# Optimization experiments

Measured on AMD Instinct MI355X. Metric: run time of the kernel, lower is better.

Reference implementation:

```python
import jax, jax.numpy as jnp
import numpy as np

B, N, D, H, P = 8, 1025, 768, 12, 32  # n = P*P + 1 (CLS + patches)
HD = D // H
EPS = 1e-5


def setup_inputs() -> dict:
    key = jax.random.key(0)
    ks = jax.random.split(key, 6)
    return {
        "x": jax.random.normal(ks[0], (B, N, D), dtype=jnp.float32),
        "canny": jax.random.uniform(ks[1], (B, 1, P, P), dtype=jnp.float32),
        "noise": jax.random.uniform(ks[2], (B, P, P), dtype=jnp.float32),
        "ln_w": jnp.ones((D,), dtype=jnp.float32),
        "ln_b": jnp.zeros((D,), dtype=jnp.float32),
        "w_qkv": (jax.random.normal(ks[3], (D, 3 * D), dtype=jnp.float32) * 0.02),
        "w_out": (jax.random.normal(ks[4], (D, D), dtype=jnp.float32) * 0.02),
        "b_out": jnp.zeros((D,), dtype=jnp.float32),
    }


def reference(x, canny, noise, ln_w, ln_b, w_qkv, w_out, b_out):
    b, n, d = x.shape
    # LayerNorm
    mu = jnp.mean(x, axis=-1, keepdims=True)
    var = jnp.mean(jnp.square(x - mu), axis=-1, keepdims=True)
    x_norm = (x - mu) * jax.lax.rsqrt(var + EPS) * ln_w + ln_b
    # QKV projection (no bias), split into heads: [b, n, 3, h, hd]
    qkv = (x_norm @ w_qkv).reshape(b, n, 3, H, HD)
    q = jnp.transpose(qkv[:, :, 0], (0, 2, 1, 3))  # [b, h, n, hd]
    k = jnp.transpose(qkv[:, :, 1], (0, 2, 1, 3))
    v = jnp.transpose(qkv[:, :, 2], (0, 2, 1, 3))
    # NOTE: source uses scale = dim ** -0.5 (full dim, not head_dim)
    dots = jnp.einsum('bhid,bhjd->bhij', q, k) * (d ** -0.5)
    # CLS-row prior injection: softmax over patch keys of CLS query row
    attn_row = jax.nn.softmax(dots[:, :, 0, 1:], axis=-1)  # [b, h, n-1]
    canny_flat = canny.reshape(b, -1) + 1.0                # [b, n-1]
    canny_flat = canny_flat / jnp.sum(canny_flat, axis=-1, keepdims=True)
    noise_flat = noise.reshape(b, -1)                      # [b, n-1]
    noise_flat = noise_flat / jnp.sum(noise_flat, axis=-1, keepdims=True)
    attn_row = attn_row + canny_flat[:, None, :] + noise_flat[:, None, :]
    dots = dots.at[:, :, 0, 1:].set(attn_row)
    # Second (full) softmax; dropout is identity in eval mode
    attn = jax.nn.softmax(dots, axis=-1)
    out = jnp.einsum('bhij,bhjd->bhid', attn, v)           # [b, h, n, hd]
    out = jnp.transpose(out, (0, 2, 1, 3)).reshape(b, n, d)
    return out @ w_out + b_out
```

## Files before the change

### kernel.cpp

```cpp
#include <hip/hip_runtime.h>

#define B_ 8
#define N_ 1025
#define D_ 768
#define H_ 12
#define NP_ 1024
#define ROWS_ (B_*N_)
#define ROWS_PAD_ 8320
#define QKVC_ 2304
#define SCALE_ 0.03608439182435161f
#define EPS_ 1e-5f

typedef float f32x4 __attribute__((ext_vector_type(4)));
typedef short s16x8 __attribute__((ext_vector_type(8)));

#define GLD16(g, l) __builtin_amdgcn_global_load_lds( \
    (const __attribute__((address_space(1))) unsigned int*)(g), \
    (__attribute__((address_space(3))) unsigned int*)(l), 16, 0, 0)

__device__ __forceinline__ float blo(unsigned int u){
  union { unsigned int i; float f; } v; v.i = u << 16; return v.f;
}
__device__ __forceinline__ float bhi(unsigned int u){
  union { unsigned int i; float f; } v; v.i = u & 0xffff0000u; return v.f;
}
__device__ __forceinline__ float bf2f(unsigned short u){
  union { unsigned int i; float f; } v; v.i = ((unsigned int)u) << 16; return v.f;
}
__device__ __forceinline__ unsigned short f2bf(float f){
  union { unsigned int i; float f; } v; v.f = f;
  unsigned int b = v.i;
  b = b + 0x7fffu + ((b >> 16) & 1u);
  return (unsigned short)(b >> 16);
}
__device__ __forceinline__ unsigned int pkbf2(float a, float b){
  union { float f; unsigned int i; } ua, ub;
  ua.f = a; ub.f = b;
  return __builtin_amdgcn_perm(ub.i + 0x8000u, ua.i + 0x8000u, 0x07060302u);
}

__global__ __launch_bounds__(256) void prep_fused(
    const float* __restrict__ w1, unsigned short* __restrict__ d1,
    const float* __restrict__ w2, unsigned short* __restrict__ d2,
    const float* __restrict__ x, const float* __restrict__ lw,
    const float* __restrict__ lb, unsigned short* __restrict__ xn) {
  int id = blockIdx.x;
  int t = threadIdx.x;
  if (id < 2304) {
    __shared__ unsigned short tile[32][33];
    int bx = id % 96;
    int kb = (id / 96) * 32;
    const float* src; unsigned short* dst; int N, nb;
    if (bx < 72) { src = w1; dst = d1; N = QKVC_; nb = bx * 32; }
    else         { src = w2; dst = d2; N = D_;    nb = (bx - 72) * 32; }
    int tx = t & 31, ty = t >> 5;
    #pragma unroll
    for (int i = 0; i < 4; i++) {
      int r = ty + i * 8;
      tile[r][tx] = f2bf(src[(size_t)(kb + r) * N + nb + tx]);
    }
    __syncthreads();
    #pragma unroll
    for (int i = 0; i < 4; i++) {
      int r = ty + i * 8;
      dst[(size_t)(nb + r) * D_ + kb + tx] = tile[tx][r];
    }
  } else {
    int row = id - 2304;
    __shared__ float r6[6];
    float4 v; float s = 0.f, q = 0.f;
    if (t < 192) {
      v = ((const float4*)(x + (size_t)row * D_))[t];
      s = v.x + v.y + v.z + v.w;
      q = v.x * v.x + v.y * v.y + v.z * v.z + v.w * v.w;
      #pragma unroll
      for (int off = 32; off > 0; off >>= 1) {
        s += __shfl_xor(s, off, 64);
        q += __shfl_xor(q, off, 64);
      }
      if ((t & 63) == 0) { r6[t >> 6] = s; r6[3 + (t >> 6)] = q; }
    }
    __syncthreads();
    if (t < 192) {
      s = r6[0] + r6[1] + r6[2];
      q = r6[3] + r6[4] + r6[5];
      float mean = s * (1.0f / 768.0f);
      float var = q * (1.0f / 768.0f) - mean * mean;
      var = var < 0.f ? 0.f : var;
      float rstd = rsqrtf(var + EPS_);
      float4 wv4 = ((const float4*)lw)[t];
      float4 bv4 = ((const float4*)lb)[t];
      float o0 = (v.x - mean) * rstd * wv4.x + bv4.x;
      float o1 = (v.y - mean) * rstd * wv4.y + bv4.y;
      float o2 = (v.z - mean) * rstd * wv4.z + bv4.z;
      float o3 = (v.w - mean) * rstd * wv4.w + bv4.w;
      uint2 pk = {pkbf2(o0, o1), pkbf2(o2, o3)};
      *(uint2*)(xn + (size_t)row * D_ + t * 4) = pk;
    }
  }
}

template <bool OF32>
__global__ __launch_bounds__(256) void gemm_bt(
    const unsigned short* __restrict__ A, const unsigned short* __restrict__ Bt,
    void* __restrict__ Cv, const float* __restrict__ bias,
    int Mvalid, int Nn, int Kk) {
  __shared__ short sh[32768];
  int t = threadIdx.x;
  int lane = t & 63, w = t >> 6;
  int m16 = lane & 15, quad = lane >> 4;

  int nwg = gridDim.x;
  int nbx = Nn >> 7;
  int id = blockIdx.x;
  int qq = nwg >> 3, rr = nwg & 7;
  int xcd = id & 7, off = id >> 3;
  int wg = (xcd < rr ? xcd * (qq + 1) : rr * (qq + 1) + (xcd - rr) * qq) + off;
  int bx = wg % nbx, by = wg / nbx;
  int bm = by * 128, bn = bx * 128;

  int wm = (w & 1) * 64, wn = (w >> 1) * 64;

  f32x4 acc[4][4];
  #pragma unroll
  for (int i = 0; i < 4; i++)
    #pragma unroll
    for (int j = 0; j < 4; j++) acc[i][j] = (f32x4){0.f, 0.f, 0.f, 0.f};

  const unsigned short* aP[4];
  const unsigned short* bP[4];
  #pragma unroll
  for (int c = 0; c < 4; c++) {
    int g = t + c * 256;
    int row = g >> 3, slot = g & 7;
    aP[c] = A  + (size_t)(bm + row) * Kk + ((slot ^ (row & 7)) * 8);
    bP[c] = Bt + (size_t)(bn + row) * Kk + ((slot ^ (row & 7)) * 8);
  }

  int KS = Kk >> 6;
  int cur = 0;
  #pragma unroll
  for (int c = 0; c < 4; c++) GLD16(aP[c], sh + (t + c * 256) * 8);
  #pragma unroll
  for (int c = 0; c < 4; c++) GLD16(bP[c], sh + 16384 + (t + c * 256) * 8);

  for (int kt = 0; kt < KS; kt++) {
    asm volatile("s_waitcnt vmcnt(0)" ::: "memory");
    __builtin_amdgcn_s_barrier();
    if (kt + 1 < KS) {
      int nb2 = (cur ^ 1) * 8192;
      int ko = (kt + 1) * 64;
      #pragma unroll
      for (int c = 0; c < 4; c++) GLD16(aP[c] + ko, sh + nb2 + (t + c * 256) * 8);
      #pragma unroll
      for (int c = 0; c < 4; c++) GLD16(bP[c] + ko, sh + 16384 + nb2 + (t + c * 256) * 8);
    }
    const short* sa = sh + cur * 8192;
    const short* sb = sh + 16384 + cur * 8192;
    #pragma unroll
    for (int ks = 0; ks < 2; ks++) {
      int so = ((ks * 4 + quad) ^ (m16 & 7)) * 8;
      s16x8 af[4], bfr[4];
      #pragma unroll
      for (int i = 0; i < 4; i++) {
        af[i]  = *(const s16x8*)(sa + (wm + i * 16 + m16) * 64 + so);
        bfr[i] = *(const s16x8*)(sb + (wn + i * 16 + m16) * 64 + so);
      }
      __builtin_amdgcn_s_setprio(1);
      #pragma unroll
      for (int i = 0; i < 4; i++)
        #pragma unroll
        for (int j = 0; j < 4; j++)
          acc[i][j] = __builtin_amdgcn_mfma_f32_16x16x32_bf16(af[i], bfr[j], acc[i][j], 0, 0, 0);
      __builtin_amdgcn_s_setprio(0);
    }
    cur ^= 1;
  }
  __syncthreads();

  if (!OF32) {
    unsigned short* C = (unsigned short*)Cv;
    #pragma unroll
    for (int j = 0; j < 4; j++) {
      int col = wn + j * 16 + m16;
      #pragma unroll
      for (int i = 0; i < 4; i++)
        #pragma unroll
        for (int r = 0; r < 4; r++)
          sh[(wm + i * 16 + quad * 4 + r) * 128 + col] = (short)f2bf(acc[i][j][r]);
    }
    __syncthreads();
    #pragma unroll
    for (int c = 0; c < 8; c++) {
      int idx = c * 256 + t;
      int row = idx >> 4, col = (idx & 15) * 8;
      if (bm + row < Mvalid)
        *(uint4*)(&C[(size_t)(bm + row) * Nn + bn + col]) = *(const uint4*)(&sh[row * 128 + col]);
    }
  } else {
    float* Cf = (float*)Cv;
    float* shf = (float*)sh;
    #pragma unroll
    for (int j = 0; j < 4; j++) {
      int col = wn + j * 16 + m16;
      float bv = bias ? bias[bn + col] : 0.f;
      #pragma unroll
      for (int i = 0; i < 4; i++)
        #pragma unroll
        for (int r = 0; r < 4; r++)
          shf[(wm + i * 16 + quad * 4 + r) * 128 + col] = acc[i][j][r] + bv;
    }
    __syncthreads();
    #pragma unroll
    for (int c = 0; c < 16; c++) {
      int idx = c * 256 + t;
      int row = idx >> 5, col = (idx & 31) * 4;
      if (bm + row < Mvalid)
        *(float4*)(&Cf[(size_t)(bm + row) * Nn + bn + col]) =
            *(const float4*)(&shf[row * 128 + col]);
    }
  }
}

__device__ __forceinline__ float block_sum(float v, float* red) {
  int t = threadIdx.x;
  red[t] = v;
  __syncthreads();
  for (int st = 128; st > 0; st >>= 1) {
    if (t < st) red[t] += red[t + st];
    __syncthreads();
  }
  float r = red[0];
  __syncthreads();
  return r;
}

__global__ __launch_bounds__(256) void attn_fused(
    const unsigned short* __restrict__ qkv, const float* __restrict__ canny,
    const float* __restrict__ noise, unsigned short* __restrict__ attn_out) {
  __shared__ __align__(16) char pool[37888];
  int id = blockIdx.x;
  int t = threadIdx.x;

  if (id < 768) {
    short* ps = (short*)pool;
    short* ks = (short*)(pool + 18432);
    unsigned int* vs = (unsigned int*)(pool + 27648);
    float* tailbuf = (float*)(pool + 36864);

    int tile = id / 96;
    int rem = id % 96;
    int h = rem >> 3;
    int b = rem & 7;
    int lane = t & 63, w = t >> 6;
    int m16 = lane & 15, quad = lane >> 4;

    int qbase = 1 + tile * 128;

    {
      int r = t >> 1, seg = (t & 1) * 32;
      const uint4* src = (const uint4*)(qkv + (size_t)(b * N_ + qbase + r) * QKVC_ + h * 64 + seg);
      uint4 u0 = src[0], u1 = src[1], u2 = src[2], u3 = src[3];
      *(uint4*)(&ps[r * 72 + seg])      = u0;
      *(uint4*)(&ps[r * 72 + seg + 8])  = u1;
      *(uint4*)(&ps[r * 72 + seg + 16]) = u2;
      *(uint4*)(&ps[r * 72 + seg + 24]) = u3;
    }
    s16x8 qb[2][2];
    #pragma unroll
    for (int nt = 0; nt < 2; nt++)
      #pragma unroll
      for (int ks_ = 0; ks_ < 2; ks_++) {
        qb[nt][ks_] = *(const s16x8*)(&ps[(w * 32 + nt * 16 + m16) * 72 + ks_ * 32 + quad * 8]);
        unsigned int* u = (unsigned int*)&qb[nt][ks_];
        #pragma unroll
        for (int i = 0; i < 4; i++)
          u[i] = pkbf2(blo(u[i]) * SCALE_, bhi(u[i]) * SCALE_);
      }
    s16x8 vone;
    #pragma unroll
    for (int i = 0; i < 8; i++) vone[i] = (short)0x3F80;

    f32x4 oacc[2][4], lacc[2];
    #pragma unroll
    for (int mt = 0; mt < 2; mt++) {
      lacc[mt] = (f32x4){0.f, 0.f, 0.f, 0.f};
      #pragma unroll
      for (int dt = 0; dt < 4; dt++) oacc[mt][dt] = (f32x4){0.f, 0.f, 0.f, 0.f};
    }

    int kkey = t >> 2, kseg = (t & 3) * 16;
    const unsigned short* kbase = qkv + (size_t)(b * N_) * QKVC_ + D_ + h * 64;
    int vp2 = t & 31, vseg = t >> 5;
    const unsigned short* vbase = qkv + (size_t)(b * N_) * QKVC_ + 2 * D_ + h * 64 + vseg * 8;
    uint4 kr0, kr1, vr0, vr1;
    {
      const uint4* ksrc = (const uint4*)(kbase + (size_t)kkey * QKVC_ + kseg);
      kr0 = ksrc[0]; kr1 = ksrc[1];
      vr0 = *(const uint4*)(vbase + (size_t)(2 * vp2) * QKVC_);
      vr1 = *(const uint4*)(vbase + (size_t)(2 * vp2 + 1) * QKVC_);
    }

    for (int jt = 0; jt < 16; jt++) {
      __syncthreads();
      *(uint4*)(&ks[kkey * 72 + kseg])     = kr0;
      *(uint4*)(&ks[kkey * 72 + kseg + 8]) = kr1;
      {
        const unsigned int* vaw = (const unsigned int*)&vr0;
        const unsigned int* vbw = (const unsigned int*)&vr1;
        #pragma unroll
        for (int i = 0; i < 4; i++) {
          vs[(vseg * 8 + 2 * i)     * 36 + vp2] = __builtin_amdgcn_perm(vbw[i], vaw[i], 0x05040100u);
          vs[(vseg * 8 + 2 * i + 1) * 36 + vp2] = __builtin_amdgcn_perm(vbw[i], vaw[i], 0x07060302u);
        }
      }
      __syncthreads();
      if (jt < 15) {
        int j0 = (jt + 1) * 64;
        const uint4* ksrc = (const uint4*)(kbase + (size_t)(j0 + kkey) * QKVC_ + kseg);
        kr0 = ksrc[0]; kr1 = ksrc[1];
        vr0 = *(const uint4*)(vbase + (size_t)(j0 + 2 * vp2) * QKVC_);
        vr1 = *(const uint4*)(vbase + (size_t)(j0 + 2 * vp2 + 1) * QKVC_);
      }
      f32x4 sacc[4][2];
      #pragma unroll
      for (int kt = 0; kt < 4; kt++) {
        s16x8 ka0 = *(const s16x8*)(&ks[(kt * 16 + m16) * 72 + quad * 8]);
        s16x8 ka1 = *(const s16x8*)(&ks[(kt * 16 + m16) * 72 + 32 + quad * 8]);
        #pragma unroll
        for (int nt = 0; nt < 2; nt++) {
          f32x4 s = (f32x4){0.f, 0.f, 0.f, 0.f};
          s = __builtin_amdgcn_mfma_f32_16x16x32_bf16(ka0, qb[nt][0], s, 0, 0, 0);
          s = __builtin_amdgcn_mfma_f32_16x16x32_bf16(ka1, qb[nt][1], s, 0, 0, 0);
          sacc[kt][nt] = s;
        }
      }
      #pragma unroll
      for (int kt = 0; kt < 4; kt++) {
        #pragma unroll
        for (int nt = 0; nt < 2; nt++) {
          f32x4 s = sacc[kt][nt];
          float p0 = __expf(s[0]);
          float p1 = __expf(s[1]);
          float p2 = __expf(s[2]);
          float p3 = __expf(s[3]);
          uint2 pk = {pkbf2(p0, p1), pkbf2(p2, p3)};
          *(uint2*)(&ps[(w * 32 + nt * 16 + m16) * 72 + kt * 16 + quad * 4]) = pk;
        }
      }
      __syncthreads();
      s16x8 pa[2][2];
      #pragma unroll
      for (int mt = 0; mt < 2; mt++)
        #pragma unroll
        for (int ks_ = 0; ks_ < 2; ks_++)
          pa[mt][ks_] = *(const s16x8*)(&ps[(w * 32 + mt * 16 + m16) * 72 + ks_ * 32 + quad * 8]);
      const short* vss = (const short*)vs;
      #pragma unroll
      for (int dt = 0; dt < 4; dt++) {
        s16x8 vb0 = *(const s16x8*)(&vss[(dt * 16 + m16) * 72 + quad * 8]);
        s16x8 vb1 = *(const s16x8*)(&vss[(dt * 16 + m16) * 72 + 32 + quad * 8]);
        #pragma unroll
        for (int mt = 0; mt < 2; mt++) {
          oacc[mt][dt] = __builtin_amdgcn_mfma_f32_16x16x32_bf16(pa[mt][0], vb0, oacc[mt][dt], 0, 0, 0);
          oacc[mt][dt] = __builtin_amdgcn_mfma_f32_16x16x32_bf16(pa[mt][1], vb1, oacc[mt][dt], 0, 0, 0);
        }
      }
      #pragma unroll
      for (int mt = 0; mt < 2; mt++) {
        lacc[mt] = __builtin_amdgcn_mfma_f32_16x16x32_bf16(pa[mt][0], vone, lacc[mt], 0, 0, 0);
        lacc[mt] = __builtin_amdgcn_mfma_f32_16x16x32_bf16(pa[mt][1], vone, lacc[mt], 0, 0, 0);
      }
    }
    if (t < 64)       tailbuf[t]             = bf2f(qkv[(size_t)(b * N_ + 1024) * QKVC_ + D_     + h * 64 + t]);
    else if (t < 128) tailbuf[64 + (t - 64)] = bf2f(qkv[(size_t)(b * N_ + 1024) * QKVC_ + 2 * D_ + h * 64 + (t - 64)]);
    __syncthreads();
    #pragma unroll
    for (int nt = 0; nt < 2; nt++) {
      float d = 0.f;
      #pragma unroll
      for (int jj = 0; jj < 8; jj++) {
        d += bf2f((unsigned short)qb[nt][0][jj]) * tailbuf[quad * 8 + jj];
        d += bf2f((unsigned short)qb[nt][1][jj]) * tailbuf[32 + quad * 8 + jj];
      }
      d += __shfl_xor(d, 16, 64);
      d += __shfl_xor(d, 32, 64);
      float p = __expf(d);
      if (quad == 0) tailbuf[128 + w * 32 + nt * 16 + m16] = p;
    }
    __syncthreads();
    #pragma unroll
    for (int mt = 0; mt < 2; mt++)
      #pragma unroll
      for (int r = 0; r < 4; r++) {
        float pr = tailbuf[128 + w * 32 + mt * 16 + quad * 4 + r];
        lacc[mt][r] += pr;
        #pragma unroll
        for (int dt = 0; dt < 4; dt++)
          oacc[mt][dt][r] += pr * tailbuf[64 + dt * 16 + m16];
      }
    #pragma unroll
    for (int mt = 0; mt < 2; mt++) {
      float rinv[4];
      #pragma unroll
      for (int r = 0; r < 4; r++) rinv[r] = 1.0f / lacc[mt][r];
      #pragma unroll
      for (int dt = 0; dt < 4; dt++) {
        #pragma unroll
        for (int r = 0; r < 4; r++) {
          int grow = b * N_ + qbase + w * 32 + mt * 16 + quad * 4 + r;
          attn_out[(size_t)grow * D_ + h * 64 + dt * 16 + m16] = f2bf(oacc[mt][dt][r] * rinv[r]);
        }
      }
    }
  } else {
    float* s     = (float*)pool;
    float* red   = (float*)(pool + 4608);
    float* q     = (float*)(pool + 5632);
    float* pvred = (float*)(pool + 5888);

    int bh = id - 768;
    int b = bh / H_, h = bh % H_;

    if (t < 64) q[t] = bf2f(qkv[(size_t)(b * N_) * QKVC_ + h * 64 + t]);
    __syncthreads();

    for (int j = t; j < N_; j += 256) {
      const unsigned short* krow = qkv + (size_t)(b * N_ + j) * QKVC_ + D_ + h * 64;
      float dot = 0.f;
      #pragma unroll
      for (int c = 0; c < 8; c++) {
        uint4 kk = *(const uint4*)(krow + c * 8);
        dot += q[c*8+0]*blo(kk.x) + q[c*8+1]*bhi(kk.x)
             + q[c*8+2]*blo(kk.y) + q[c*8+3]*bhi(kk.y)
             + q[c*8+4]*blo(kk.z) + q[c*8+5]*bhi(kk.z)
             + q[c*8+6]*blo(kk.w) + q[c*8+7]*bhi(kk.w);
      }
      s[j] = dot * SCALE_;
    }
    float cp = 0.f, npp = 0.f;
    for (int j = t; j < NP_; j += 256) {
      cp  += canny[b * NP_ + j] + 1.0f;
      npp += noise[b * NP_ + j];
    }
    float csum = block_sum(cp, red);
    float nsum = block_sum(npp, red);
    float e1 = 0.f;
    for (int j = t; j < N_; j += 256) if (j >= 1) e1 += __expf(s[j]);
    float sum1 = block_sum(e1, red);
    for (int j = t; j < N_; j += 256) {
      if (j >= 1) {
        s[j] = __expf(s[j]) / sum1
             + (canny[b * NP_ + j - 1] + 1.0f) / csum
             + noise[b * NP_ + j - 1] / nsum;
      }
    }
    __syncthreads();
    float e2 = 0.f;
    for (int j = t; j < N_; j += 256) { float e = __expf(s[j]); s[j] = e; e2 += e; }
    float sum2 = block_sum(e2, red);
    {
      int o = t & 7, g = t >> 3;
      float a[8] = {0.f, 0.f, 0.f, 0.f, 0.f, 0.f, 0.f, 0.f};
      for (int j = g; j < N_; j += 32) {
        float sv = s[j];
        uint4 vv = *(const uint4*)(qkv + (size_t)(b * N_ + j) * QKVC_ + 2 * D_ + h * 64 + o * 8);
        a[0] += sv * blo(vv.x); a[1] += sv * bhi(vv.x);
        a[2] += sv * blo(vv.y); a[3] += sv * bhi(vv.y);
        a[4] += sv * blo(vv.z); a[5] += sv * bhi(vv.z);
        a[6] += sv * blo(vv.w); a[7] += sv * bhi(vv.w);
      }
      #pragma unroll
      for (int i = 0; i < 8; i++) pvred[(o * 8 + i) * 33 + g] = a[i];
    }
    __syncthreads();
    if (t < 64) {
      float acc = 0.f;
      #pragma unroll
      for (int u = 0; u < 32; u++) acc += pvred[t * 33 + u];
      attn_out[(size_t)(b * N_) * D_ + h * 64 + t] = f2bf(acc / sum2);
    }
  }
}

extern "C" void kernel_launch(void* const* d_in, const int* in_sizes, int n_in,
                              void* d_out, int out_size, void* d_ws, size_t ws_size,
                              hipStream_t stream) {
  (void)in_sizes; (void)n_in; (void)out_size; (void)ws_size;
  const float* x     = (const float*)d_in[0];
  const float* canny = (const float*)d_in[1];
  const float* noise = (const float*)d_in[2];
  const float* lnw   = (const float*)d_in[3];
  const float* lnb   = (const float*)d_in[4];
  const float* wqkv  = (const float*)d_in[5];
  const float* wout  = (const float*)d_in[6];
  const float* bout  = (const float*)d_in[7];
  float* out = (float*)d_out;
  char* ws = (char*)d_ws;

  unsigned short* xn    = (unsigned short*)(ws);
  unsigned short* wqkvT = (unsigned short*)(ws + 12779520);
  unsigned short* woutT = (unsigned short*)(ws + 16318464);
  unsigned short* qkv   = (unsigned short*)(ws + 17498112);

  prep_fused<<<dim3(2304 + ROWS_), 256, 0, stream>>>(
      wqkv, wqkvT, wout, woutT, x, lnw, lnb, xn);
  gemm_bt<false><<<dim3((QKVC_ / 128) * (ROWS_PAD_ / 128)), 256, 0, stream>>>(
      xn, wqkvT, (void*)qkv, nullptr, ROWS_, QKVC_, D_);
  attn_fused<<<dim3(768 + B_ * H_), 256, 0, stream>>>(qkv, canny, noise, xn);
  gemm_bt<true><<<dim3((D_ / 128) * (ROWS_PAD_ / 128)), 256, 0, stream>>>(
      xn, woutT, (void*)out, bout, ROWS_, D_, D_);
}
```

Measured before the change: 205.4 us.

## Widen GEMM tiles to 128x256 with 8 waves and BK=32 staging

The bf16 GEMM kernel now uses 512 threads (8 waves) computing a 128x256 output tile instead of 256 threads on 128x128. K-step staging drops from 64 to 32, with a 4-slot XOR swizzle to fit the larger B tile in a smaller LDS buffer. The epilogue is split into halves or quarters to reuse the reduced shared memory. This is meant to improve A-tile reuse and per-block MFMA density. The costs are half as many workgroups, which matters for the 768-wide output projection, and twice as many barrier iterations along K.

```diff
diff --git a/kernel.cpp b/kernel.cpp
--- a/kernel.cpp
+++ b/kernel.cpp
@@ -101,25 +101,25 @@
 }
 
 template <bool OF32>
-__global__ __launch_bounds__(256) void gemm_bt(
+__global__ __launch_bounds__(512) void gemm_bt(
     const unsigned short* __restrict__ A, const unsigned short* __restrict__ Bt,
     void* __restrict__ Cv, const float* __restrict__ bias,
     int Mvalid, int Nn, int Kk) {
-  __shared__ short sh[32768];
+  __shared__ short sh[24576];
   int t = threadIdx.x;
   int lane = t & 63, w = t >> 6;
   int m16 = lane & 15, quad = lane >> 4;
 
   int nwg = gridDim.x;
-  int nbx = Nn >> 7;
+  int nbx = Nn >> 8;
   int id = blockIdx.x;
   int qq = nwg >> 3, rr = nwg & 7;
   int xcd = id & 7, off = id >> 3;
   int wg = (xcd < rr ? xcd * (qq + 1) : rr * (qq + 1) + (xcd - rr) * qq) + off;
   int bx = wg % nbx, by = wg / nbx;
-  int bm = by * 128, bn = bx * 128;
-
-  int wm = (w & 1) * 64, wn = (w >> 1) * 64;
+  int bm = by * 128, bn = bx * 256;
+
+  int wm = (w >> 2) * 64, wn = (w & 3) * 64;
 
   f32x4 acc[4][4];
   #pragma unroll
@@ -127,97 +127,100 @@
     #pragma unroll
     for (int j = 0; j < 4; j++) acc[i][j] = (f32x4){0.f, 0.f, 0.f, 0.f};
 
-  const unsigned short* aP[4];
-  const unsigned short* bP[4];
-  #pragma unroll
-  for (int c = 0; c < 4; c++) {
-    int g = t + c * 256;
-    int row = g >> 3, slot = g & 7;
-    aP[c] = A  + (size_t)(bm + row) * Kk + ((slot ^ (row & 7)) * 8);
-    bP[c] = Bt + (size_t)(bn + row) * Kk + ((slot ^ (row & 7)) * 8);
-  }
-
-  int KS = Kk >> 6;
+  int srow = t >> 2;
+  int sxor = ((t & 3) ^ (srow & 3)) * 8;
+  const unsigned short* aP  = A  + (size_t)(bm + srow) * Kk + sxor;
+  const unsigned short* bP0 = Bt + (size_t)(bn + srow) * Kk + sxor;
+  const unsigned short* bP1 = Bt + (size_t)(bn + 128 + srow) * Kk + sxor;
+
+  int KS = Kk >> 5;
   int cur = 0;
-  #pragma unroll
-  for (int c = 0; c < 4; c++) GLD16(aP[c], sh + (t + c * 256) * 8);
-  #pragma unroll
-  for (int c = 0; c < 4; c++) GLD16(bP[c], sh + 16384 + (t + c * 256) * 8);
-
+  GLD16(aP,  sh + t * 8);
+  GLD16(bP0, sh + 4096 + t * 8);
+  GLD16(bP1, sh + 4096 + (t + 512) * 8);
+
+  int so = (quad ^ (m16 & 3)) * 8;
   for (int kt = 0; kt < KS; kt++) {
     asm volatile("s_waitcnt vmcnt(0)" ::: "memory");
     __builtin_amdgcn_s_barrier();
     if (kt + 1 < KS) {
-      int nb2 = (cur ^ 1) * 8192;
-      int ko = (kt + 1) * 64;
-      #pragma unroll
-      for (int c = 0; c < 4; c++) GLD16(aP[c] + ko, sh + nb2 + (t + c * 256) * 8);
-      #pragma unroll
-      for (int c = 0; c < 4; c++) GLD16(bP[c] + ko, sh + 16384 + nb2 + (t + c * 256) * 8);
-    }
-    const short* sa = sh + cur * 8192;
-    const short* sb = sh + 16384 + cur * 8192;
-    #pragma unroll
-    for (int ks = 0; ks < 2; ks++) {
-      int so = ((ks * 4 + quad) ^ (m16 & 7)) * 8;
-      s16x8 af[4], bfr[4];
-      #pragma unroll
-      for (int i = 0; i < 4; i++) {
-        af[i]  = *(const s16x8*)(sa + (wm + i * 16 + m16) * 64 + so);
-        bfr[i] = *(const s16x8*)(sb + (wn + i * 16 + m16) * 64 + so);
-      }
-      __builtin_amdgcn_s_setprio(1);
-      #pragma unroll
-      for (int i = 0; i < 4; i++)
-        #pragma unroll
-        for (int j = 0; j < 4; j++)
-          acc[i][j] = __builtin_amdgcn_mfma_f32_16x16x32_bf16(af[i], bfr[j], acc[i][j], 0, 0, 0);
-      __builtin_amdgcn_s_setprio(0);
-    }
+      int nb2 = (cur ^ 1) * 12288;
+      int ko = (kt + 1) * 32;
+      GLD16(aP + ko,  sh + nb2 + t * 8);
+      GLD16(bP0 + ko, sh + nb2 + 4096 + t * 8);
+      GLD16(bP1 + ko, sh + nb2 + 4096 + (t + 512) * 8);
+    }
+    const short* sa = sh + cur * 12288;
+    const short* sb = sa + 4096;
+    s16x8 af[4], bfr[4];
+    #pragma unroll
+    for (int i = 0; i < 4; i++) {
+      af[i]  = *(const s16x8*)(sa + (wm + i * 16 + m16) * 32 + so);
+      bfr[i] = *(const s16x8*)(sb + (wn + i * 16 + m16) * 32 + so);
+    }
+    __builtin_amdgcn_s_setprio(1);
+    #pragma unroll
+    for (int i = 0; i < 4; i++)
+      #pragma unroll
+      for (int j = 0; j < 4; j++)
+        acc[i][j] = __builtin_amdgcn_mfma_f32_16x16x32_bf16(af[i], bfr[j], acc[i][j], 0, 0, 0);
+    __builtin_amdgcn_s_setprio(0);
     cur ^= 1;
   }
-  __syncthreads();
 
   if (!OF32) {
     unsigned short* C = (unsigned short*)Cv;
     #pragma unroll
-    for (int j = 0; j < 4; j++) {
-      int col = wn + j * 16 + m16;
-      #pragma unroll
-      for (int i = 0; i < 4; i++)
-        #pragma unroll
-        for (int r = 0; r < 4; r++)
-          sh[(wm + i * 16 + quad * 4 + r) * 128 + col] = (short)f2bf(acc[i][j][r]);
-    }
-    __syncthreads();
-    #pragma unroll
-    for (int c = 0; c < 8; c++) {
-      int idx = c * 256 + t;
-      int row = idx >> 4, col = (idx & 15) * 8;
-      if (bm + row < Mvalid)
-        *(uint4*)(&C[(size_t)(bm + row) * Nn + bn + col]) = *(const uint4*)(&sh[row * 128 + col]);
+    for (int half = 0; half < 2; half++) {
+      __syncthreads();
+      if ((wn >> 7) == half) {
+        #pragma unroll
+        for (int j = 0; j < 4; j++) {
+          int col = (wn & 127) + j * 16 + m16;
+          #pragma unroll
+          for (int i = 0; i < 4; i++)
+            #pragma unroll
+            for (int r = 0; r < 4; r++)
+              sh[(wm + i * 16 + quad * 4 + r) * 128 + col] = (short)f2bf(acc[i][j][r]);
+        }
+      }
+      __syncthreads();
+      #pragma unroll
+      for (int c = 0; c < 4; c++) {
+        int idx = c * 512 + t;
+        int row = idx >> 4, col = (idx & 15) * 8;
+        if (bm + row < Mvalid)
+          *(uint4*)(&C[(size_t)(bm + row) * Nn + bn + half * 128 + col]) =
+              *(const uint4*)(&sh[row * 128 + col]);
+      }
     }
   } else {
     float* Cf = (float*)Cv;
     float* shf = (float*)sh;
     #pragma unroll
-    for (int j = 0; j < 4; j++) {
-      int col = wn + j * 16 + m16;
-      float bv = bias ? bias[bn + col] : 0.f;
-      #pragma unroll
-      for (int i = 0; i < 4; i++)
-        #pragma unroll
-        for (int r = 0; r < 4; r++)
-          shf[(wm + i * 16 + quad * 4 + r) * 128 + col] = acc[i][j][r] + bv;
-    }
-    __syncthreads();
-    #pragma unroll
-    for (int c = 0; c < 16; c++) {
-      int idx = c * 256 + t;
-      int row = idx >> 5, col = (idx & 31) * 4;
-      if (bm + row < Mvalid)
-        *(float4*)(&Cf[(size_t)(bm + row) * Nn + bn + col]) =
-            *(const float4*)(&shf[row * 128 + col]);
+    for (int q = 0; q < 4; q++) {
+      __syncthreads();
+      if ((wn >> 6) == q) {
+        #pragma unroll
+        for (int j = 0; j < 4; j++) {
+          int colg = bn + wn + j * 16 + m16;
+          float bv = bias ? bias[colg] : 0.f;
+          #pragma unroll
+          for (int i = 0; i < 4; i++)
+            #pragma unroll
+            for (int r = 0; r < 4; r++)
+              shf[(wm + i * 16 + quad * 4 + r) * 64 + j * 16 + m16] = acc[i][j][r] + bv;
+        }
+      }
+      __syncthreads();
+      #pragma unroll
+      for (int c = 0; c < 4; c++) {
+        int idx = c * 512 + t;
+        int row = idx >> 4, col = (idx & 15) * 4;
+        if (bm + row < Mvalid)
+          *(float4*)(&Cf[(size_t)(bm + row) * Nn + bn + q * 64 + col]) =
+              *(const float4*)(&shf[row * 64 + col]);
+      }
     }
   }
 }
@@ -505,9 +508,9 @@
 
   prep_fused<<<dim3(2304 + ROWS_), 256, 0, stream>>>(
       wqkv, wqkvT, wout, woutT, x, lnw, lnb, xn);
-  gemm_bt<false><<<dim3((QKVC_ / 128) * (ROWS_PAD_ / 128)), 256, 0, stream>>>(
+  gemm_bt<false><<<dim3((QKVC_ / 256) * (ROWS_PAD_ / 128)), 512, 0, stream>>>(
       xn, wqkvT, (void*)qkv, nullptr, ROWS_, QKVC_, D_);
   attn_fused<<<dim3(768 + B_ * H_), 256, 0, stream>>>(qkv, canny, noise, xn);
-  gemm_bt<true><<<dim3((D_ / 128) * (ROWS_PAD_ / 128)), 256, 0, stream>>>(
+  gemm_bt<true><<<dim3((D_ / 256) * (ROWS_PAD_ / 128)), 512, 0, stream>>>(
       xn, woutT, (void*)out, bout, ROWS_, D_, D_);
 }
```

After: 215.2 us. 4.8% more time.
